# Kernel tuning notes

Hardware: AMD Instinct MI355X
Metric: run time of the kernel (lower is better)

Reference implementation:

```python
import math
import jax, jax.numpy as jnp
import numpy as np

B = 8192
BAND = 5      # channels per DGCN
N = 62        # graph nodes (EEG electrodes)
LAYERS = 2
CBAM_C = (LAYERS + 1) * BAND  # 15
RED = 4
H2 = 64
K_TOP = int(N * 0.8)  # 49


def conv1x1(x, w, b):
    # x: [B,C,N,T], w: [O,C], b: [O] or None
    y = jnp.einsum('bcnt,oc->bont', x, w)
    if b is not None:
        y = y + b[None, :, None, None]
    return y


def dgcn(x, conv_w, conv_b, mem, gfc_w, gfc_b, gcn_w, gcn_b):
    skip = x
    x = conv1x1(x, conv_w, conv_b)
    scale = 1.0 / math.sqrt(BAND)
    # dynamic adjacency 1: memory-based
    a1 = jax.nn.softmax(jax.nn.relu(jnp.einsum('bcnt,cm->bnm', x, mem) * scale), axis=-1)
    # dynamic adjacency 2: self-similarity of time-summed features
    xs = jnp.sum(x, axis=-1)  # [B,C,N]
    a2 = jax.nn.softmax(jax.nn.relu(jnp.einsum('bcn,bcm->bnm', xs, xs) * scale), axis=-1)
    af = jnp.stack([a1, a2], axis=-1)          # [B,N,N,2]
    af = jnp.einsum('bnmk,ok->bnmo', af, gfc_w)[..., 0] + gfc_b[0]  # fc(2->1), squeeze
    af = jax.nn.softmax(af, axis=-1)
    _, idx = jax.lax.top_k(af, K_TOP)          # [B,N,k]
    bI = jnp.arange(af.shape[0])[:, None, None]
    nI = jnp.arange(N)[None, :, None]
    mask = jnp.zeros_like(af).at[bI, nI, idx].set(1.0)
    adj = af * mask
    # diffusion step (diffusion_step=1)
    y = jnp.einsum('bcnt,bnm->bcmt', x, adj)
    y = conv1x1(y, gcn_w, gcn_b)
    return y + skip


def cbam(x, ca_w1, ca_w2, sa_w, sa_b):
    residual = x
    # channel attention: shared SE MLP on max- and avg-pooled descriptors
    mx = jnp.max(x, axis=(2, 3), keepdims=True)   # [B,C,1,1]
    av = jnp.mean(x, axis=(2, 3), keepdims=True)
    def se(z):
        z = jnp.einsum('bcnt,oc->bont', z, ca_w1)
        z = jax.nn.relu(z)
        return jnp.einsum('bcnt,oc->bont', z, ca_w2)
    ca = jax.nn.sigmoid(se(mx) + se(av))
    out = x * ca
    # spatial attention: 3x3 conv over [max,mean] channel maps
    smax = jnp.max(out, axis=1, keepdims=True)
    smean = jnp.mean(out, axis=1, keepdims=True)
    s = jnp.concatenate([smax, smean], axis=1)    # [B,2,H,W]
    sa = jax.lax.conv_general_dilated(
        s, sa_w, window_strides=(1, 1), padding=((1, 1), (1, 1)),
        dimension_numbers=('NCHW', 'OIHW', 'NCHW')) + sa_b[None, :, None, None]
    sa = jax.nn.sigmoid(sa)
    out = out * sa
    return out + residual


def setup_inputs() -> dict:
    key = jax.random.key(0)
    ks = jax.random.split(key, 24)
    p = {}
    p['x'] = jax.random.normal(ks[0], (B, BAND * N), dtype=jnp.float32)
    for l in range(LAYERS):
        o = 1 + l * 8
        p[f'l{l}_conv_w'] = jax.random.normal(ks[o + 0], (BAND, BAND), jnp.float32) * 0.3
        p[f'l{l}_conv_b'] = jnp.zeros((BAND,), jnp.float32)
        p[f'l{l}_mem'] = jax.random.normal(ks[o + 1], (BAND, N), jnp.float32) * 0.2
        p[f'l{l}_gfc_w'] = jax.random.normal(ks[o + 2], (1, 2), jnp.float32) * 0.5
        p[f'l{l}_gfc_b'] = jnp.zeros((1,), jnp.float32)
        p[f'l{l}_gcn_w'] = jax.random.normal(ks[o + 3], (BAND, BAND), jnp.float32) * 0.3
        p[f'l{l}_gcn_b'] = jnp.zeros((BAND,), jnp.float32)
    p['ca_w1'] = jax.random.normal(ks[17], (CBAM_C // RED, CBAM_C), jnp.float32) * 0.2
    p['ca_w2'] = jax.random.normal(ks[18], (CBAM_C, CBAM_C // RED), jnp.float32) * 0.2
    p['sa_w'] = jax.random.normal(ks[19], (1, 2, 3, 3), jnp.float32) * 0.2
    p['sa_b'] = jnp.zeros((1,), jnp.float32)
    p['fc1_w'] = jax.random.normal(ks[20], (H2, N * CBAM_C), jnp.float32) * 0.03
    p['fc1_b'] = jnp.zeros((H2,), jnp.float32)
    p['fc2_w'] = jax.random.normal(ks[21], (H2, H2), jnp.float32) * 0.1
    p['fc2_b'] = jnp.zeros((H2,), jnp.float32)
    return p


def reference(x,
              l0_conv_w, l0_conv_b, l0_mem, l0_gfc_w, l0_gfc_b, l0_gcn_w, l0_gcn_b,
              l1_conv_w, l1_conv_b, l1_mem, l1_gfc_w, l1_gfc_b, l1_gcn_w, l1_gcn_b,
              ca_w1, ca_w2, sa_w, sa_b, fc1_w, fc1_b, fc2_w, fc2_b):
    h = x.reshape(x.shape[0], BAND, N)[:, :, :, None]  # [B,5,62,1]
    feats = [h]
    layer_params = [
        (l0_conv_w, l0_conv_b, l0_mem, l0_gfc_w, l0_gfc_b, l0_gcn_w, l0_gcn_b),
        (l1_conv_w, l1_conv_b, l1_mem, l1_gfc_w, l1_gfc_b, l1_gcn_w, l1_gcn_b),
    ]
    cur = h
    for lp in layer_params:
        cur = dgcn(cur, *lp)
        feats.append(cur)
    g = jnp.concatenate(feats, axis=1)                 # [B,15,62,1]
    g = cbam(g, ca_w1, ca_w2, sa_w, sa_b)
    out = g.reshape(g.shape[0], -1)
    out = jax.nn.relu(out @ fc1_w.T + fc1_b)           # dropout = identity (eval)
    out = jax.nn.relu(out @ fc2_w.T + fc2_b)
    return out
```

## Files before the change

### kernel.cpp

```cpp
#include <hip/hip_runtime.h>

#define NB 62
#define NC 5
#define KTOP 49

typedef unsigned short ushort_t;
typedef unsigned int uint_t;

__device__ __forceinline__ float sigmf(float x) {
    return 1.0f / (1.0f + __expf(-x));
}

__device__ __forceinline__ ushort_t f2b(float f) {
    union { float f; uint_t u; } cv; cv.f = f;
    uint_t r = (cv.u + 0x7fffu + ((cv.u >> 16) & 1u)) >> 16;
    return (ushort_t)r;
}
__device__ __forceinline__ float b2f(ushort_t h) {
    union { uint_t u; float f; } cv; cv.u = ((uint_t)h) << 16;
    return cv.f;
}
__device__ __forceinline__ float blo(uint_t w) {
    union { uint_t u; float f; } cv; cv.u = w << 16; return cv.f;
}
__device__ __forceinline__ float bhi(uint_t w) {
    union { uint_t u; float f; } cv; cv.u = w & 0xffff0000u; return cv.f;
}

__device__ __forceinline__ float tmax62(const float* a) {
    float t0 = a[0], t1 = a[1], t2 = a[2], t3 = a[3];
    #pragma unroll
    for (int m = 4; m < 60; m += 4) {
        t0 = fmaxf(t0, a[m]);     t1 = fmaxf(t1, a[m + 1]);
        t2 = fmaxf(t2, a[m + 2]); t3 = fmaxf(t3, a[m + 3]);
    }
    t0 = fmaxf(t0, a[60]); t1 = fmaxf(t1, a[61]);
    return fmaxf(fmaxf(t0, t1), fmaxf(t2, t3));
}
__device__ __forceinline__ float tsum62(const float* a) {
    float t0 = a[0], t1 = a[1], t2 = a[2], t3 = a[3];
    #pragma unroll
    for (int m = 4; m < 60; m += 4) {
        t0 += a[m]; t1 += a[m + 1]; t2 += a[m + 2]; t3 += a[m + 3];
    }
    t0 += a[60]; t1 += a[61];
    return (t0 + t1) + (t2 + t3);
}

__global__ void repack_kernel(const float* __restrict__ fc1w,
                              const float* __restrict__ fc2w,
                              ushort_t* __restrict__ w1o,
                              float* __restrict__ w2o) {
    const int i = blockIdx.x * 256 + threadIdx.x;
    if (i < 117 * 64 * 8) {
        const int j = i & 7, o = (i >> 3) & 63, i8 = i >> 9;
        const int src = i8 * 8 + j;
        const float v = (src < 930) ? fc1w[o * 930 + src] : 0.0f;
        w1o[i] = f2b(v);
    } else if (i < 117 * 64 * 8 + 16 * 64 * 4) {
        const int i2 = i - 117 * 64 * 8;
        const int j = i2 & 3, o = (i2 >> 2) & 63, k4 = i2 >> 8;
        w2o[i2] = fc2w[o * 64 + k4 * 4 + j];
    }
}

__global__ void __launch_bounds__(64) __attribute__((amdgpu_waves_per_eu(2, 3)))
encoder_kernel(
    const float* __restrict__ g_x,
    const float* __restrict__ c0w, const float* __restrict__ c0b,
    const float* __restrict__ m0,  const float* __restrict__ f0w,
    const float* __restrict__ f0b, const float* __restrict__ g0w,
    const float* __restrict__ g0b,
    const float* __restrict__ c1w, const float* __restrict__ c1b,
    const float* __restrict__ m1,  const float* __restrict__ f1w,
    const float* __restrict__ f1b, const float* __restrict__ g1w,
    const float* __restrict__ g1b,
    const float* __restrict__ caw1, const float* __restrict__ caw2,
    const float* __restrict__ saw,  const float* __restrict__ sab,
    const float* __restrict__ fc1w, const float* __restrict__ fc1b,
    const float* __restrict__ fc2w, const float* __restrict__ fc2b,
    const ushort_t* __restrict__ w1b, const float* __restrict__ w2p,
    const int use_ws,
    float* __restrict__ g_out)
{
    const int b   = blockIdx.x;
    const int tid = threadIdx.x;

    __shared__ __align__(16) ushort_t s_adjh[NB * 66];
    __shared__ __align__(16) float s_xm[NB][12];
    __shared__ float s_xt[3][NB][NC];
    __shared__ float s_mx[16], s_av[16], s_ca[16];
    __shared__ float s_smax[64], s_smean[64];
    __shared__ __align__(16) float s_h1[64];

    float* s_g = (float*)s_adjh;

    for (int i = tid; i < NC * NB; i += 64) {
        const int c = i / NB, n = i - c * NB;
        s_xt[0][n][c] = g_x[(size_t)b * (NC * NB) + i];
    }
    __syncthreads();

    const float scale = 0.44721359549995793f;

    for (int l = 0; l < 2; ++l) {
        const float* conv_w = l ? c1w : c0w;
        const float* conv_b = l ? c1b : c0b;
        const float* memp   = l ? m1  : m0;
        const float* gfc_w  = l ? f1w : f0w;
        const float* gfc_b  = l ? f1b : f0b;
        const float* gcn_w  = l ? g1w : g0w;
        const float* gcn_b  = l ? g1b : g0b;

        for (int i = tid; i < NC * NB; i += 64) {
            const int c = i / NB, m = i - c * NB;
            s_xm[m][c < 4 ? 4 + c : 9] = memp[i];
        }

        float cw[25], cb[5], gw[25], gb[5];
        #pragma unroll
        for (int i = 0; i < 25; ++i) cw[i] = conv_w[i];
        #pragma unroll
        for (int i = 0; i < 5; ++i)  cb[i] = conv_b[i];
        #pragma unroll
        for (int i = 0; i < 25; ++i) gw[i] = gcn_w[i];
        #pragma unroll
        for (int i = 0; i < 5; ++i)  gb[i] = gcn_b[i];
        const float w0 = gfc_w[0], w1 = gfc_w[1], b0 = gfc_b[0];

        float xo0 = 0, xo1 = 0, xo2 = 0, xo3 = 0, xo4 = 0;
        if (tid < NB) {
            const int n = tid;
            float xn[5];
            #pragma unroll
            for (int c = 0; c < 5; ++c) xn[c] = s_xt[l][n][c];
            xo0 = cb[0]; xo1 = cb[1]; xo2 = cb[2]; xo3 = cb[3]; xo4 = cb[4];
            #pragma unroll
            for (int c = 0; c < 5; ++c) {
                xo0 = fmaf(cw[0 * 5 + c], xn[c], xo0);
                xo1 = fmaf(cw[1 * 5 + c], xn[c], xo1);
                xo2 = fmaf(cw[2 * 5 + c], xn[c], xo2);
                xo3 = fmaf(cw[3 * 5 + c], xn[c], xo3);
                xo4 = fmaf(cw[4 * 5 + c], xn[c], xo4);
            }
            s_xm[n][0] = xo0; s_xm[n][1] = xo1; s_xm[n][2] = xo2;
            s_xm[n][3] = xo3; s_xm[n][8] = xo4;
        }
        __syncthreads();

        if (tid < NB) {
            float r1[NB];
            float r2[64];
            #pragma unroll
            for (int m = 0; m < NB; ++m) {
                const float4 xc03 = *(const float4*)&s_xm[m][0];
                const float4 me03 = *(const float4*)&s_xm[m][4];
                const float2 t45  = *(const float2*)&s_xm[m][8];
                float s1 = xo0 * me03.x + xo1 * me03.y + xo2 * me03.z + xo3 * me03.w + xo4 * t45.y;
                float s2 = xo0 * xc03.x + xo1 * xc03.y + xo2 * xc03.z + xo3 * xc03.w + xo4 * t45.x;
                r1[m] = fmaxf(s1 * scale, 0.0f);
                r2[m] = fmaxf(s2 * scale, 0.0f);
            }
            const float mx1 = tmax62(r1);
            #pragma unroll
            for (int m = 0; m < NB; ++m) r1[m] = __expf(r1[m] - mx1);
            const float inv1 = 1.0f / tsum62(r1);
            const float mx2 = tmax62(r2);
            #pragma unroll
            for (int m = 0; m < NB; ++m) r2[m] = __expf(r2[m] - mx2);
            const float inv2 = 1.0f / tsum62(r2);
            #pragma unroll
            for (int m = 0; m < NB; ++m)
                r1[m] = b0 + (r1[m] * inv1) * w0 + (r2[m] * inv2) * w1;
            const float mxa = tmax62(r1);
            #pragma unroll
            for (int m = 0; m < NB; ++m) r1[m] = __expf(r1[m] - mxa);
            const float inva = 1.0f / tsum62(r1);
            #pragma unroll
            for (int m = 0; m < NB; ++m) r1[m] *= inva;

            #pragma unroll
            for (int m = 0; m < NB; ++m) r2[m] = r1[m];
            r2[62] = INFINITY; r2[63] = INFINITY;
            #pragma unroll
            for (int k = 2; k <= 64; k <<= 1) {
                #pragma unroll
                for (int j = k >> 1; j > 0; j >>= 1) {
                    #pragma unroll
                    for (int i = 0; i < 64; ++i) {
                        const int p = i ^ j;
                        if (p > i) {
                            const bool up = ((i & k) == 0);
                            const float a = r2[i], c = r2[p];
                            r2[i] = up ? fminf(a, c) : fmaxf(a, c);
                            r2[p] = up ? fmaxf(a, c) : fminf(a, c);
                        }
                    }
                }
            }
            const float vth = r2[13];

            int gc0 = 0, gc1 = 0, gc2 = 0, gc3 = 0;
            #pragma unroll
            for (int m = 0; m < 60; m += 4) {
                gc0 += (r1[m] > vth);     gc1 += (r1[m + 1] > vth);
                gc2 += (r1[m + 2] > vth); gc3 += (r1[m + 3] > vth);
            }
            gc0 += (r1[60] > vth); gc1 += (r1[61] > vth);
            const int G = (gc0 + gc1) + (gc2 + gc3);
            int eq = 0;
            const int n = tid;
            #pragma unroll
            for (int m = 0; m < NB; ++m) {
                const bool e  = (r1[m] == vth);
                const bool ss = (r1[m] > vth) || (e && (G + eq) < KTOP);
                s_adjh[n * 66 + m] = f2b(ss ? r1[m] : 0.0f);
                eq += e ? 1 : 0;
            }
        }
        __syncthreads();

        if (tid < NB) {
            const int m = tid;
            float y0 = 0, y1 = 0, y2 = 0, y3 = 0, y4 = 0;
            for (int n = 0; n < NB; ++n) {
                const float a = b2f(s_adjh[n * 66 + m]);
                const float4 xv = *(const float4*)&s_xm[n][0];
                const float  xv4 = s_xm[n][8];
                y0 = fmaf(xv.x, a, y0); y1 = fmaf(xv.y, a, y1); y2 = fmaf(xv.z, a, y2);
                y3 = fmaf(xv.w, a, y3); y4 = fmaf(xv4, a, y4);
            }
            #pragma unroll
            for (int o = 0; o < 5; ++o) {
                const float z = gb[o] + gw[o * 5 + 0] * y0 + gw[o * 5 + 1] * y1 +
                                gw[o * 5 + 2] * y2 + gw[o * 5 + 3] * y3 + gw[o * 5 + 4] * y4;
                s_xt[l + 1][m][o] = z + s_xt[l][m][o];
            }
        }
        __syncthreads();
    }

    if (tid < 15) {
        const int lidx = tid / 5, cc = tid - lidx * 5;
        float mxv = -INFINITY, sm = 0.0f;
        for (int n = 0; n < NB; ++n) {
            const float v = s_xt[lidx][n][cc];
            mxv = fmaxf(mxv, v);
            sm += v;
        }
        s_mx[tid] = mxv;
        s_av[tid] = sm * (1.0f / 62.0f);
    }
    __syncthreads();
    if (tid < 15) {
        float t = 0.0f;
        #pragma unroll
        for (int o = 0; o < 3; ++o) {
            float am = 0.0f, aa = 0.0f;
            #pragma unroll
            for (int c = 0; c < 15; ++c) {
                const float w = caw1[o * 15 + c];
                am = fmaf(s_mx[c], w, am);
                aa = fmaf(s_av[c], w, aa);
            }
            t = fmaf(fmaxf(am, 0.0f) + fmaxf(aa, 0.0f), caw2[tid * 3 + o], t);
        }
        s_ca[tid] = sigmf(t);
    }
    __syncthreads();
    float og[15];
    if (tid < NB) {
        const int n = tid;
        float smx = -INFINITY, ssum = 0.0f;
        #pragma unroll
        for (int c = 0; c < 15; ++c) {
            const int lidx = c / 5, cc = c - lidx * 5;
            const float v = s_xt[lidx][n][cc] * s_ca[c];
            og[c] = v;
            smx = fmaxf(smx, v);
            ssum += v;
        }
        s_smax[n]  = smx;
        s_smean[n] = ssum * (1.0f / 15.0f);
    }
    __syncthreads();
    if (tid < NB) {
        const int n = tid;
        float t = sab[0];
        #pragma unroll
        for (int kh = 0; kh < 3; ++kh) {
            const int nn = n - 1 + kh;
            const int ncl = nn < 0 ? 0 : (nn > NB - 1 ? NB - 1 : nn);
            const float msk = (nn >= 0 && nn < NB) ? 1.0f : 0.0f;
            t += msk * (s_smax[ncl] * saw[kh * 3 + 1] + s_smean[ncl] * saw[9 + kh * 3 + 1]);
        }
        const float sa = sigmf(t);
        #pragma unroll
        for (int c = 0; c < 15; ++c) {
            const int lidx = c / 5, cc = c - lidx * 5;
            s_g[c * NB + n] = og[c] * sa + s_xt[lidx][n][cc];
        }
    }
    if (tid < 6) s_g[930 + tid] = 0.0f;
    __syncthreads();

    if (use_ws) {
        float acc = fc1b[tid];
        const uint4* w1v = (const uint4*)w1b;
        #pragma unroll 4
        for (int i8 = 0; i8 < 117; ++i8) {
            const uint4 wv = w1v[i8 * 64 + tid];
            const float4 ga = *(const float4*)&s_g[i8 * 8];
            const float4 gb2 = *(const float4*)&s_g[i8 * 8 + 4];
            acc = fmaf(blo(wv.x), ga.x,  acc);
            acc = fmaf(bhi(wv.x), ga.y,  acc);
            acc = fmaf(blo(wv.y), ga.z,  acc);
            acc = fmaf(bhi(wv.y), ga.w,  acc);
            acc = fmaf(blo(wv.z), gb2.x, acc);
            acc = fmaf(bhi(wv.z), gb2.y, acc);
            acc = fmaf(blo(wv.w), gb2.z, acc);
            acc = fmaf(bhi(wv.w), gb2.w, acc);
        }
        s_h1[tid] = fmaxf(acc, 0.0f);
        __syncthreads();
        float acc2 = fc2b[tid];
        #pragma unroll
        for (int k4 = 0; k4 < 16; ++k4) {
            const float4 wv = *(const float4*)(w2p + k4 * 256 + tid * 4);
            const float4 hv = *(const float4*)&s_h1[k4 * 4];
            acc2 = fmaf(wv.x, hv.x, acc2);
            acc2 = fmaf(wv.y, hv.y, acc2);
            acc2 = fmaf(wv.z, hv.z, acc2);
            acc2 = fmaf(wv.w, hv.w, acc2);
        }
        g_out[(size_t)b * 64 + tid] = fmaxf(acc2, 0.0f);
    } else {
        float acc = fc1b[tid];
        const float* wr = fc1w + (size_t)tid * 930;
        #pragma unroll 4
        for (int i = 0; i < 928; i += 2) {
            const float2 wv = *(const float2*)(wr + i);
            const float2 gv = *(const float2*)(&s_g[i]);
            acc = fmaf(wv.x, gv.x, fmaf(wv.y, gv.y, acc));
        }
        acc += wr[928] * s_g[928] + wr[929] * s_g[929];
        s_h1[tid] = fmaxf(acc, 0.0f);
        __syncthreads();
        float acc2 = fc2b[tid];
        const float* wr2 = fc2w + tid * 64;
        #pragma unroll
        for (int k = 0; k < 64; k += 4) {
            const float4 wv = *(const float4*)(wr2 + k);
            acc2 = fmaf(wv.x, s_h1[k], acc2);
            acc2 = fmaf(wv.y, s_h1[k + 1], acc2);
            acc2 = fmaf(wv.z, s_h1[k + 2], acc2);
            acc2 = fmaf(wv.w, s_h1[k + 3], acc2);
        }
        g_out[(size_t)b * 64 + tid] = fmaxf(acc2, 0.0f);
    }
}

extern "C" void kernel_launch(void* const* d_in, const int* in_sizes, int n_in,
                              void* d_out, int out_size, void* d_ws, size_t ws_size,
                              hipStream_t stream) {
    const float* X    = (const float*)d_in[0];
    const float* C0W  = (const float*)d_in[1];
    const float* C0B  = (const float*)d_in[2];
    const float* M0   = (const float*)d_in[3];
    const float* F0W  = (const float*)d_in[4];
    const float* F0B  = (const float*)d_in[5];
    const float* G0W  = (const float*)d_in[6];
    const float* G0B  = (const float*)d_in[7];
    const float* C1W  = (const float*)d_in[8];
    const float* C1B  = (const float*)d_in[9];
    const float* M1   = (const float*)d_in[10];
    const float* F1W  = (const float*)d_in[11];
    const float* F1B  = (const float*)d_in[12];
    const float* G1W  = (const float*)d_in[13];
    const float* G1B  = (const float*)d_in[14];
    const float* CAW1 = (const float*)d_in[15];
    const float* CAW2 = (const float*)d_in[16];
    const float* SAW  = (const float*)d_in[17];
    const float* SAB  = (const float*)d_in[18];
    const float* FC1W = (const float*)d_in[19];
    const float* FC1B = (const float*)d_in[20];
    const float* FC2W = (const float*)d_in[21];
    const float* FC2B = (const float*)d_in[22];

    const int B = in_sizes[0] / (NC * NB);

    const size_t W1_BYTES = 117 * 64 * 8 * sizeof(ushort_t);
    const size_t W2_BYTES = 16 * 64 * 4 * sizeof(float);
    const int use_ws = (ws_size >= W1_BYTES + W2_BYTES) ? 1 : 0;
    ushort_t* w1b = (ushort_t*)d_ws;
    float*    w2p = (float*)((char*)d_ws + W1_BYTES);

    if (use_ws) {
        repack_kernel<<<250, 256, 0, stream>>>(FC1W, FC2W, w1b, w2p);
    }

    encoder_kernel<<<B, 64, 0, stream>>>(
        X, C0W, C0B, M0, F0W, F0B, G0W, G0B,
        C1W, C1B, M1, F1W, F1B, G1W, G1B,
        CAW1, CAW2, SAW, SAB, FC1W, FC1B, FC2W, FC2B,
        w1b, w2p, use_ws,
        (float*)d_out);
}
```

Measured before the change: 250.4 us.

## Keep per-node features in registers and use wave shuffles for CBAM reductions

Per-node layer features now stay in per-thread registers instead of a shared-memory feature array, and the DGCN layer is split out into an inlined helper. The CBAM channel max/mean pooling is done with 64-lane xor shuffles, and the spatial 3-tap conv uses shuffle up/down, which removes several shared-memory round trips and __syncthreads barriers. Every thread computes all 15 channel-attention values redundantly, and the extra live registers may hurt occupancy. The gcn weights are also now loaded later in each layer.

```diff
diff --git a/kernel.cpp b/kernel.cpp
--- a/kernel.cpp
+++ b/kernel.cpp
@@ -62,6 +62,142 @@
         const int j = i2 & 3, o = (i2 >> 2) & 63, k4 = i2 >> 8;
         w2o[i2] = fc2w[o * 64 + k4 * 4 + j];
     }
+}
+
+__device__ __forceinline__ void dgcn_layer(
+    const int tid,
+    const float* __restrict__ fin, float* __restrict__ fout,
+    const float* __restrict__ conv_w, const float* __restrict__ conv_b,
+    const float* __restrict__ memp,
+    const float* __restrict__ gfc_w, const float* __restrict__ gfc_b,
+    const float* __restrict__ gcn_w, const float* __restrict__ gcn_b,
+    ushort_t* __restrict__ s_adjh, float (*__restrict__ s_xm)[12])
+{
+    const float scale = 0.44721359549995793f;
+
+    for (int i = tid; i < NC * NB; i += 64) {
+        const int c = i / NB, m = i - c * NB;
+        s_xm[m][c < 4 ? 4 + c : 9] = memp[i];
+    }
+
+    float cw[25], cb[5];
+    #pragma unroll
+    for (int i = 0; i < 25; ++i) cw[i] = conv_w[i];
+    #pragma unroll
+    for (int i = 0; i < 5; ++i)  cb[i] = conv_b[i];
+    const float w0 = gfc_w[0], w1 = gfc_w[1], b0 = gfc_b[0];
+
+    float xo0 = 0, xo1 = 0, xo2 = 0, xo3 = 0, xo4 = 0;
+    if (tid < NB) {
+        xo0 = cb[0]; xo1 = cb[1]; xo2 = cb[2]; xo3 = cb[3]; xo4 = cb[4];
+        #pragma unroll
+        for (int c = 0; c < 5; ++c) {
+            const float xn = fin[c];
+            xo0 = fmaf(cw[c],      xn, xo0);
+            xo1 = fmaf(cw[5 + c],  xn, xo1);
+            xo2 = fmaf(cw[10 + c], xn, xo2);
+            xo3 = fmaf(cw[15 + c], xn, xo3);
+            xo4 = fmaf(cw[20 + c], xn, xo4);
+        }
+        s_xm[tid][0] = xo0; s_xm[tid][1] = xo1; s_xm[tid][2] = xo2;
+        s_xm[tid][3] = xo3; s_xm[tid][8] = xo4;
+    }
+    __syncthreads();
+
+    if (tid < NB) {
+        float r1[NB];
+        float r2[64];
+        #pragma unroll
+        for (int m = 0; m < NB; ++m) {
+            const float4 xc03 = *(const float4*)&s_xm[m][0];
+            const float4 me03 = *(const float4*)&s_xm[m][4];
+            const float2 t45  = *(const float2*)&s_xm[m][8];
+            float s1 = xo0 * me03.x + xo1 * me03.y + xo2 * me03.z + xo3 * me03.w + xo4 * t45.y;
+            float s2 = xo0 * xc03.x + xo1 * xc03.y + xo2 * xc03.z + xo3 * xc03.w + xo4 * t45.x;
+            r1[m] = fmaxf(s1 * scale, 0.0f);
+            r2[m] = fmaxf(s2 * scale, 0.0f);
+        }
+        const float mx1 = tmax62(r1);
+        #pragma unroll
+        for (int m = 0; m < NB; ++m) r1[m] = __expf(r1[m] - mx1);
+        const float inv1 = 1.0f / tsum62(r1);
+        const float mx2 = tmax62(r2);
+        #pragma unroll
+        for (int m = 0; m < NB; ++m) r2[m] = __expf(r2[m] - mx2);
+        const float inv2 = 1.0f / tsum62(r2);
+        #pragma unroll
+        for (int m = 0; m < NB; ++m)
+            r1[m] = b0 + (r1[m] * inv1) * w0 + (r2[m] * inv2) * w1;
+        const float mxa = tmax62(r1);
+        #pragma unroll
+        for (int m = 0; m < NB; ++m) r1[m] = __expf(r1[m] - mxa);
+        const float inva = 1.0f / tsum62(r1);
+        #pragma unroll
+        for (int m = 0; m < NB; ++m) r1[m] *= inva;
+
+        #pragma unroll
+        for (int m = 0; m < NB; ++m) r2[m] = r1[m];
+        r2[62] = INFINITY; r2[63] = INFINITY;
+        #pragma unroll
+        for (int k = 2; k <= 64; k <<= 1) {
+            #pragma unroll
+            for (int j = k >> 1; j > 0; j >>= 1) {
+                #pragma unroll
+                for (int i = 0; i < 64; ++i) {
+                    const int p = i ^ j;
+                    if (p > i) {
+                        const bool up = ((i & k) == 0);
+                        const float a = r2[i], c = r2[p];
+                        r2[i] = up ? fminf(a, c) : fmaxf(a, c);
+                        r2[p] = up ? fmaxf(a, c) : fminf(a, c);
+                    }
+                }
+            }
+        }
+        const float vth = r2[13];
+
+        int gc0 = 0, gc1 = 0, gc2 = 0, gc3 = 0;
+        #pragma unroll
+        for (int m = 0; m < 60; m += 4) {
+            gc0 += (r1[m] > vth);     gc1 += (r1[m + 1] > vth);
+            gc2 += (r1[m + 2] > vth); gc3 += (r1[m + 3] > vth);
+        }
+        gc0 += (r1[60] > vth); gc1 += (r1[61] > vth);
+        const int G = (gc0 + gc1) + (gc2 + gc3);
+        int eq = 0;
+        #pragma unroll
+        for (int m = 0; m < NB; ++m) {
+            const bool e  = (r1[m] == vth);
+            const bool ss = (r1[m] > vth) || (e && (G + eq) < KTOP);
+            s_adjh[tid * 66 + m] = f2b(ss ? r1[m] : 0.0f);
+            eq += e ? 1 : 0;
+        }
+    }
+    __syncthreads();
+
+    if (tid < NB) {
+        const int m = tid;
+        float y0 = 0, y1 = 0, y2 = 0, y3 = 0, y4 = 0;
+        for (int n = 0; n < NB; ++n) {
+            const float a = b2f(s_adjh[n * 66 + m]);
+            const float4 xv = *(const float4*)&s_xm[n][0];
+            const float  xv4 = s_xm[n][8];
+            y0 = fmaf(xv.x, a, y0); y1 = fmaf(xv.y, a, y1); y2 = fmaf(xv.z, a, y2);
+            y3 = fmaf(xv.w, a, y3); y4 = fmaf(xv4, a, y4);
+        }
+        float gw[25], gb[5];
+        #pragma unroll
+        for (int i = 0; i < 25; ++i) gw[i] = gcn_w[i];
+        #pragma unroll
+        for (int i = 0; i < 5; ++i)  gb[i] = gcn_b[i];
+        #pragma unroll
+        for (int o = 0; o < 5; ++o) {
+            const float z = gb[o] + gw[o * 5 + 0] * y0 + gw[o * 5 + 1] * y1 +
+                            gw[o * 5 + 2] * y2 + gw[o * 5 + 3] * y3 + gw[o * 5 + 4] * y4;
+            fout[o] = z + fin[o];
+        }
+    }
+    __syncthreads();
 }
 
 __global__ void __launch_bounds__(64) __attribute__((amdgpu_waves_per_eu(2, 3)))
@@ -88,217 +224,82 @@
 
     __shared__ __align__(16) ushort_t s_adjh[NB * 66];
     __shared__ __align__(16) float s_xm[NB][12];
-    __shared__ float s_xt[3][NB][NC];
-    __shared__ float s_mx[16], s_av[16], s_ca[16];
-    __shared__ float s_smax[64], s_smean[64];
-    __shared__ __align__(16) float s_h1[64];
-
-    float* s_g = (float*)s_adjh;
-
-    for (int i = tid; i < NC * NB; i += 64) {
-        const int c = i / NB, n = i - c * NB;
-        s_xt[0][n][c] = g_x[(size_t)b * (NC * NB) + i];
-    }
-    __syncthreads();
-
-    const float scale = 0.44721359549995793f;
-
-    for (int l = 0; l < 2; ++l) {
-        const float* conv_w = l ? c1w : c0w;
-        const float* conv_b = l ? c1b : c0b;
-        const float* memp   = l ? m1  : m0;
-        const float* gfc_w  = l ? f1w : f0w;
-        const float* gfc_b  = l ? f1b : f0b;
-        const float* gcn_w  = l ? g1w : g0w;
-        const float* gcn_b  = l ? g1b : g0b;
-
-        for (int i = tid; i < NC * NB; i += 64) {
-            const int c = i / NB, m = i - c * NB;
-            s_xm[m][c < 4 ? 4 + c : 9] = memp[i];
-        }
-
-        float cw[25], cb[5], gw[25], gb[5];
-        #pragma unroll
-        for (int i = 0; i < 25; ++i) cw[i] = conv_w[i];
-        #pragma unroll
-        for (int i = 0; i < 5; ++i)  cb[i] = conv_b[i];
-        #pragma unroll
-        for (int i = 0; i < 25; ++i) gw[i] = gcn_w[i];
-        #pragma unroll
-        for (int i = 0; i < 5; ++i)  gb[i] = gcn_b[i];
-        const float w0 = gfc_w[0], w1 = gfc_w[1], b0 = gfc_b[0];
-
-        float xo0 = 0, xo1 = 0, xo2 = 0, xo3 = 0, xo4 = 0;
-        if (tid < NB) {
-            const int n = tid;
-            float xn[5];
-            #pragma unroll
-            for (int c = 0; c < 5; ++c) xn[c] = s_xt[l][n][c];
-            xo0 = cb[0]; xo1 = cb[1]; xo2 = cb[2]; xo3 = cb[3]; xo4 = cb[4];
-            #pragma unroll
-            for (int c = 0; c < 5; ++c) {
-                xo0 = fmaf(cw[0 * 5 + c], xn[c], xo0);
-                xo1 = fmaf(cw[1 * 5 + c], xn[c], xo1);
-                xo2 = fmaf(cw[2 * 5 + c], xn[c], xo2);
-                xo3 = fmaf(cw[3 * 5 + c], xn[c], xo3);
-                xo4 = fmaf(cw[4 * 5 + c], xn[c], xo4);
-            }
-            s_xm[n][0] = xo0; s_xm[n][1] = xo1; s_xm[n][2] = xo2;
-            s_xm[n][3] = xo3; s_xm[n][8] = xo4;
-        }
-        __syncthreads();
-
-        if (tid < NB) {
-            float r1[NB];
-            float r2[64];
-            #pragma unroll
-            for (int m = 0; m < NB; ++m) {
-                const float4 xc03 = *(const float4*)&s_xm[m][0];
-                const float4 me03 = *(const float4*)&s_xm[m][4];
-                const float2 t45  = *(const float2*)&s_xm[m][8];
-                float s1 = xo0 * me03.x + xo1 * me03.y + xo2 * me03.z + xo3 * me03.w + xo4 * t45.y;
-                float s2 = xo0 * xc03.x + xo1 * xc03.y + xo2 * xc03.z + xo3 * xc03.w + xo4 * t45.x;
-                r1[m] = fmaxf(s1 * scale, 0.0f);
-                r2[m] = fmaxf(s2 * scale, 0.0f);
-            }
-            const float mx1 = tmax62(r1);
-            #pragma unroll
-            for (int m = 0; m < NB; ++m) r1[m] = __expf(r1[m] - mx1);
-            const float inv1 = 1.0f / tsum62(r1);
-            const float mx2 = tmax62(r2);
-            #pragma unroll
-            for (int m = 0; m < NB; ++m) r2[m] = __expf(r2[m] - mx2);
-            const float inv2 = 1.0f / tsum62(r2);
-            #pragma unroll
-            for (int m = 0; m < NB; ++m)
-                r1[m] = b0 + (r1[m] * inv1) * w0 + (r2[m] * inv2) * w1;
-            const float mxa = tmax62(r1);
-            #pragma unroll
-            for (int m = 0; m < NB; ++m) r1[m] = __expf(r1[m] - mxa);
-            const float inva = 1.0f / tsum62(r1);
-            #pragma unroll
-            for (int m = 0; m < NB; ++m) r1[m] *= inva;
-
-            #pragma unroll
-            for (int m = 0; m < NB; ++m) r2[m] = r1[m];
-            r2[62] = INFINITY; r2[63] = INFINITY;
-            #pragma unroll
-            for (int k = 2; k <= 64; k <<= 1) {
-                #pragma unroll
-                for (int j = k >> 1; j > 0; j >>= 1) {
-                    #pragma unroll
-                    for (int i = 0; i < 64; ++i) {
-                        const int p = i ^ j;
-                        if (p > i) {
-                            const bool up = ((i & k) == 0);
-                            const float a = r2[i], c = r2[p];
-                            r2[i] = up ? fminf(a, c) : fmaxf(a, c);
-                            r2[p] = up ? fmaxf(a, c) : fminf(a, c);
-                        }
-                    }
-                }
-            }
-            const float vth = r2[13];
-
-            int gc0 = 0, gc1 = 0, gc2 = 0, gc3 = 0;
-            #pragma unroll
-            for (int m = 0; m < 60; m += 4) {
-                gc0 += (r1[m] > vth);     gc1 += (r1[m + 1] > vth);
-                gc2 += (r1[m + 2] > vth); gc3 += (r1[m + 3] > vth);
-            }
-            gc0 += (r1[60] > vth); gc1 += (r1[61] > vth);
-            const int G = (gc0 + gc1) + (gc2 + gc3);
-            int eq = 0;
-            const int n = tid;
-            #pragma unroll
-            for (int m = 0; m < NB; ++m) {
-                const bool e  = (r1[m] == vth);
-                const bool ss = (r1[m] > vth) || (e && (G + eq) < KTOP);
-                s_adjh[n * 66 + m] = f2b(ss ? r1[m] : 0.0f);
-                eq += e ? 1 : 0;
-            }
-        }
-        __syncthreads();
-
-        if (tid < NB) {
-            const int m = tid;
-            float y0 = 0, y1 = 0, y2 = 0, y3 = 0, y4 = 0;
-            for (int n = 0; n < NB; ++n) {
-                const float a = b2f(s_adjh[n * 66 + m]);
-                const float4 xv = *(const float4*)&s_xm[n][0];
-                const float  xv4 = s_xm[n][8];
-                y0 = fmaf(xv.x, a, y0); y1 = fmaf(xv.y, a, y1); y2 = fmaf(xv.z, a, y2);
-                y3 = fmaf(xv.w, a, y3); y4 = fmaf(xv4, a, y4);
-            }
-            #pragma unroll
-            for (int o = 0; o < 5; ++o) {
-                const float z = gb[o] + gw[o * 5 + 0] * y0 + gw[o * 5 + 1] * y1 +
-                                gw[o * 5 + 2] * y2 + gw[o * 5 + 3] * y3 + gw[o * 5 + 4] * y4;
-                s_xt[l + 1][m][o] = z + s_xt[l][m][o];
-            }
-        }
-        __syncthreads();
-    }
-
-    if (tid < 15) {
-        const int lidx = tid / 5, cc = tid - lidx * 5;
-        float mxv = -INFINITY, sm = 0.0f;
-        for (int n = 0; n < NB; ++n) {
-            const float v = s_xt[lidx][n][cc];
-            mxv = fmaxf(mxv, v);
-            sm += v;
-        }
-        s_mx[tid] = mxv;
-        s_av[tid] = sm * (1.0f / 62.0f);
-    }
-    __syncthreads();
-    if (tid < 15) {
-        float t = 0.0f;
+
+    float* const s_g  = (float*)s_adjh;
+    float* const s_h1 = ((float*)s_adjh) + 936;
+
+    float f0[5], f1[5] = {0, 0, 0, 0, 0}, f2[5] = {0, 0, 0, 0, 0};
+    #pragma unroll
+    for (int c = 0; c < 5; ++c)
+        f0[c] = (tid < NB) ? g_x[(size_t)b * (NC * NB) + c * NB + tid] : 0.0f;
+
+    dgcn_layer(tid, f0, f1, c0w, c0b, m0, f0w, f0b, g0w, g0b, s_adjh, s_xm);
+    dgcn_layer(tid, f1, f2, c1w, c1b, m1, f1w, f1b, g1w, g1b, s_adjh, s_xm);
+
+    float mxp[15], avp[15];
+    #pragma unroll
+    for (int c = 0; c < 15; ++c) {
+        const float v = (c < 5) ? f0[c] : (c < 10) ? f1[c - 5] : f2[c - 10];
+        float vm = (tid < NB) ? v : -INFINITY;
+        float vs = (tid < NB) ? v : 0.0f;
+        #pragma unroll
+        for (int off = 32; off > 0; off >>= 1) {
+            vm = fmaxf(vm, __shfl_xor(vm, off, 64));
+            vs += __shfl_xor(vs, off, 64);
+        }
+        mxp[c] = vm;
+        avp[c] = vs * (1.0f / 62.0f);
+    }
+    float ca[15];
+    {
+        float hm[3], ha[3];
         #pragma unroll
         for (int o = 0; o < 3; ++o) {
             float am = 0.0f, aa = 0.0f;
             #pragma unroll
             for (int c = 0; c < 15; ++c) {
                 const float w = caw1[o * 15 + c];
-                am = fmaf(s_mx[c], w, am);
-                aa = fmaf(s_av[c], w, aa);
+                am = fmaf(mxp[c], w, am);
+                aa = fmaf(avp[c], w, aa);
             }
-            t = fmaf(fmaxf(am, 0.0f) + fmaxf(aa, 0.0f), caw2[tid * 3 + o], t);
-        }
-        s_ca[tid] = sigmf(t);
-    }
-    __syncthreads();
+            hm[o] = fmaxf(am, 0.0f);
+            ha[o] = fmaxf(aa, 0.0f);
+        }
+        #pragma unroll
+        for (int c = 0; c < 15; ++c) {
+            float t = 0.0f;
+            #pragma unroll
+            for (int o = 0; o < 3; ++o) t = fmaf(hm[o] + ha[o], caw2[c * 3 + o], t);
+            ca[c] = sigmf(t);
+        }
+    }
     float og[15];
-    if (tid < NB) {
-        const int n = tid;
-        float smx = -INFINITY, ssum = 0.0f;
-        #pragma unroll
-        for (int c = 0; c < 15; ++c) {
-            const int lidx = c / 5, cc = c - lidx * 5;
-            const float v = s_xt[lidx][n][cc] * s_ca[c];
-            og[c] = v;
-            smx = fmaxf(smx, v);
-            ssum += v;
-        }
-        s_smax[n]  = smx;
-        s_smean[n] = ssum * (1.0f / 15.0f);
-    }
+    float smx = -INFINITY, ssum = 0.0f;
+    #pragma unroll
+    for (int c = 0; c < 15; ++c) {
+        const float fv = (c < 5) ? f0[c] : (c < 10) ? f1[c - 5] : f2[c - 10];
+        const float v = fv * ca[c];
+        og[c] = v;
+        smx = fmaxf(smx, v);
+        ssum += v;
+    }
+    const float smean = ssum * (1.0f / 15.0f);
+    const float sxl = __shfl_up(smx, 1, 64),   sml = __shfl_up(smean, 1, 64);
+    const float sxr = __shfl_down(smx, 1, 64), smr = __shfl_down(smean, 1, 64);
+    const float mskL = (tid > 0) ? 1.0f : 0.0f;
+    const float mskR = (tid < NB - 1) ? 1.0f : 0.0f;
+    float t = sab[0];
+    t += mskL * (sxl * saw[1] + sml * saw[10]);
+    t += smx * saw[4] + smean * saw[13];
+    t += mskR * (sxr * saw[7] + smr * saw[16]);
+    const float sa = sigmf(t);
+
     __syncthreads();
     if (tid < NB) {
-        const int n = tid;
-        float t = sab[0];
-        #pragma unroll
-        for (int kh = 0; kh < 3; ++kh) {
-            const int nn = n - 1 + kh;
-            const int ncl = nn < 0 ? 0 : (nn > NB - 1 ? NB - 1 : nn);
-            const float msk = (nn >= 0 && nn < NB) ? 1.0f : 0.0f;
-            t += msk * (s_smax[ncl] * saw[kh * 3 + 1] + s_smean[ncl] * saw[9 + kh * 3 + 1]);
-        }
-        const float sa = sigmf(t);
         #pragma unroll
         for (int c = 0; c < 15; ++c) {
-            const int lidx = c / 5, cc = c - lidx * 5;
-            s_g[c * NB + n] = og[c] * sa + s_xt[lidx][n][cc];
+            const float fv = (c < 5) ? f0[c] : (c < 10) ? f1[c - 5] : f2[c - 10];
+            s_g[c * NB + tid] = og[c] * sa + fv;
         }
     }
     if (tid < 6) s_g[930 + tid] = 0.0f;
@@ -310,7 +311,7 @@
         #pragma unroll 4
         for (int i8 = 0; i8 < 117; ++i8) {
             const uint4 wv = w1v[i8 * 64 + tid];
-            const float4 ga = *(const float4*)&s_g[i8 * 8];
+            const float4 ga  = *(const float4*)&s_g[i8 * 8];
             const float4 gb2 = *(const float4*)&s_g[i8 * 8 + 4];
             acc = fmaf(blo(wv.x), ga.x,  acc);
             acc = fmaf(bhi(wv.x), ga.y,  acc);
```

After: 274.7 us. 9.7% more time.
